# Kernel optimization log

Hardware: AMD Instinct MI355X
Metric: run time of the kernel (lower is better)

## Reference

```python
import jax, jax.numpy as jnp
import numpy as np

V = 6890      # SMPL vertex count
JNT = 24      # SMPL joints
NB = 10       # shape betas
PF = 207      # pose-blend features = 23*9
NJ_OUT = 19   # cocoplus joints
PARENTS = np.array([0, 0, 0, 0, 1, 2, 3, 4, 5, 6, 7, 8, 9, 9, 9, 12, 13, 14, 16, 17, 18, 19, 20, 21], dtype=np.int32)


def setup_inputs() -> dict:
    key = jax.random.key(0)
    ks = jax.random.split(key, 8)
    B = 512
    beta = jax.random.normal(ks[0], (B, NB), dtype=jnp.float32)
    theta = jax.random.normal(ks[1], (B, JNT * 3), dtype=jnp.float32)
    v_template = jax.random.normal(ks[2], (V, 3), dtype=jnp.float32)
    shapedirs = jax.random.normal(ks[3], (NB, V * 3), dtype=jnp.float32) * 0.01
    J_regressor = jax.random.uniform(ks[4], (V, JNT), dtype=jnp.float32)
    J_regressor = J_regressor / jnp.sum(J_regressor, axis=0, keepdims=True)
    posedirs = jax.random.normal(ks[5], (PF, V * 3), dtype=jnp.float32) * 0.01
    lbs_weights = jax.random.uniform(ks[6], (V, JNT), dtype=jnp.float32)
    lbs_weights = lbs_weights / jnp.sum(lbs_weights, axis=1, keepdims=True)
    joint_regressor = jax.random.uniform(ks[7], (V, NJ_OUT), dtype=jnp.float32)
    joint_regressor = joint_regressor / jnp.sum(joint_regressor, axis=0, keepdims=True)
    return {
        "beta": beta, "theta": theta, "v_template": v_template,
        "shapedirs": shapedirs, "J_regressor": J_regressor,
        "posedirs": posedirs, "lbs_weights": lbs_weights,
        "joint_regressor": joint_regressor,
    }


def batch_rodrigues(aa):
    # aa: [N,3] axis-angle -> [N,3,3] rotation via unit quaternion
    angle = jnp.linalg.norm(aa + 1e-8, axis=1, keepdims=True)  # [N,1]
    axis = aa / angle
    half = angle * 0.5
    w = jnp.cos(half)[:, 0]
    xyz = axis * jnp.sin(half)
    x, y, z = xyz[:, 0], xyz[:, 1], xyz[:, 2]
    w2, x2, y2, z2 = w * w, x * x, y * y, z * z
    wx, wy, wz = w * x, w * y, w * z
    xy, xz, yz = x * y, x * z, y * z
    R = jnp.stack([
        w2 + x2 - y2 - z2, 2 * (xy - wz), 2 * (xz + wy),
        2 * (xy + wz), w2 - x2 + y2 - z2, 2 * (yz - wx),
        2 * (xz - wy), 2 * (yz + wx), w2 - x2 - y2 + z2,
    ], axis=1).reshape(-1, 3, 3)
    return R


def _make_A(R, t):
    # R: [B,3,3], t: [B,3] -> [B,4,4]
    B = R.shape[0]
    top = jnp.concatenate([R, t[:, :, None]], axis=2)          # [B,3,4]
    bot = jnp.broadcast_to(jnp.array([0., 0., 0., 1.], R.dtype), (B, 1, 4))
    return jnp.concatenate([top, bot], axis=1)


def global_rigid_transform(Rs, J):
    # Rs: [B,24,3,3], J: [B,24,3]; kinematic-chain FK
    results = [_make_A(Rs[:, 0], J[:, 0])]
    for i in range(1, JNT):
        t = J[:, i] - J[:, PARENTS[i]]
        results.append(results[PARENTS[i]] @ _make_A(Rs[:, i], t))
    A = jnp.stack(results, axis=1)                              # [B,24,4,4]
    J_transformed = A[:, :, :3, 3]
    # remove rest-pose joint translation: A - [0 | A @ [J;0]]
    J_homo = jnp.concatenate([J, jnp.zeros_like(J[:, :, :1])], axis=2)  # [B,24,4]
    init_bone = jnp.einsum('bjpq,bjq->bjp', A, J_homo)          # [B,24,4]
    A_rel = A - jnp.concatenate(
        [jnp.zeros(A.shape[:3] + (3,), A.dtype), init_bone[..., None]], axis=-1)
    return J_transformed, A_rel


def reference(beta, theta, v_template, shapedirs, J_regressor, posedirs,
              lbs_weights, joint_regressor):
    B = beta.shape[0]
    # shape blend
    v_shaped = (beta @ shapedirs).reshape(B, V, 3) + v_template   # [B,V,3]
    # rest-pose joints
    J = jnp.einsum('bvc,vj->bjc', v_shaped, J_regressor)          # [B,24,3]
    # pose rotations
    Rs = batch_rodrigues(theta.reshape(-1, 3)).reshape(B, JNT, 3, 3)
    pose_feature = (Rs[:, 1:] - jnp.eye(3, dtype=Rs.dtype)).reshape(B, PF)
    v_posed = (pose_feature @ posedirs).reshape(B, V, 3) + v_shaped
    # FK
    _, A = global_rigid_transform(Rs, J)                          # [B,24,4,4]
    # skinning
    T = jnp.einsum('vj,bjpq->bvpq', lbs_weights, A)               # [B,V,4,4]
    v_homo = jnp.concatenate(
        [v_posed, jnp.ones((B, V, 1), v_posed.dtype)], axis=2)    # [B,V,4]
    verts = jnp.einsum('bvpq,bvq->bvp', T[:, :, :3, :], v_homo)   # [B,V,3]
    joints = jnp.einsum('bvc,vj->bjc', verts, joint_regressor)    # [B,19,3]
    return joints
```

## Files before the change

### kernel.cpp

```cpp
#include <hip/hip_runtime.h>
#include <math.h>

#define NV 6890
#define N3 20670
#define NJNT 24
#define NBETA 10
#define NPF 207
#define NJO 19
#define NBATCH 512
#define NJK 456
#define NJKP 512
#define NCOEF 218
#define PROWSP 768
#define KPAD 6912
#define KSPLIT 12
#define KCH 576
#define CSTR 224
#define CSTRV 6912

#define TR2 54
#define RODB 48
#define SJB 264
#define C4R 1728
#define PMV 1479
#define PMP 763
#define CHB 48
#define CMB (NJKP * C4R / 256)
#define D4R 219
#define RSP 2
#define RCH 109
#define SSTRIDE ((size_t)NBATCH * 3 * NJK)

typedef __attribute__((ext_vector_type(8))) short bfx8;
typedef __attribute__((ext_vector_type(4))) float fx4;

#define LDSP(x) ((__attribute__((address_space(3))) void*)(x))
#define GLBP(x) ((const __attribute__((address_space(1))) void*)(x))

__constant__ int d_par[NJNT] = {0,0,0,0,1,2,3,4,5,6,7,8,9,9,9,12,13,14,16,17,18,19,20,21};
__constant__ int d_path[NJNT][9] = {
  {0,-1,-1,-1,-1,-1,-1,-1,-1},
  {0,1,-1,-1,-1,-1,-1,-1,-1},
  {0,2,-1,-1,-1,-1,-1,-1,-1},
  {0,3,-1,-1,-1,-1,-1,-1,-1},
  {0,1,4,-1,-1,-1,-1,-1,-1},
  {0,2,5,-1,-1,-1,-1,-1,-1},
  {0,3,6,-1,-1,-1,-1,-1,-1},
  {0,1,4,7,-1,-1,-1,-1,-1},
  {0,2,5,8,-1,-1,-1,-1,-1},
  {0,3,6,9,-1,-1,-1,-1,-1},
  {0,1,4,7,10,-1,-1,-1,-1},
  {0,2,5,8,11,-1,-1,-1,-1},
  {0,3,6,9,12,-1,-1,-1,-1},
  {0,3,6,9,13,-1,-1,-1,-1},
  {0,3,6,9,14,-1,-1,-1,-1},
  {0,3,6,9,12,15,-1,-1,-1},
  {0,3,6,9,13,16,-1,-1,-1},
  {0,3,6,9,14,17,-1,-1,-1},
  {0,3,6,9,13,16,18,-1,-1},
  {0,3,6,9,14,17,19,-1,-1},
  {0,3,6,9,13,16,18,20,-1},
  {0,3,6,9,14,17,19,21,-1},
  {0,3,6,9,13,16,18,20,22},
  {0,3,6,9,14,17,19,21,23}};

__device__ inline short f2bf(float f) {
  union { float f; unsigned u; } x; x.f = f;
  unsigned r = (x.u + 0x7fffu + ((x.u >> 16) & 1u)) >> 16;
  return (short)r;
}

__global__ void __launch_bounds__(256) kA(const float* __restrict__ jr,
                                          const float* __restrict__ lbs,
                                          const float* __restrict__ Jreg,
                                          const float* __restrict__ sdirs,
                                          const float* __restrict__ vtmpl,
                                          const float* __restrict__ theta,
                                          const float* __restrict__ beta,
                                          const float* __restrict__ pdirs,
                                          float* __restrict__ jrT, float* __restrict__ wT,
                                          float* __restrict__ SJ, float* __restrict__ Rs,
                                          float* __restrict__ pfc,
                                          short* __restrict__ Pb) {
  __shared__ float red[4][3];
  __shared__ float tj[128 * NJO];
  __shared__ float tw[128 * NJNT];
  int bx = blockIdx.x, tid = threadIdx.x;
  if (bx < TR2) {
    int v0 = bx * 128;
    for (int i = tid; i < 128 * NJO; i += 256) {
      int g = v0 * NJO + i;
      tj[i] = (g < NV * NJO) ? jr[g] : 0.f;
    }
    for (int i = tid; i < 128 * NJNT; i += 256) {
      int g = v0 * NJNT + i;
      tw[i] = (g < NV * NJNT) ? lbs[g] : 0.f;
    }
    __syncthreads();
    for (int i = tid; i < 128 * (NJO + NJNT); i += 256) {
      int r = i >> 7, c = i & 127;
      int v = v0 + c;
      if (v >= NV) continue;
      if (r < NJO) jrT[(size_t)r * CSTRV + v] = tj[c * NJO + r];
      else         wT[(size_t)(r - NJO) * CSTRV + v] = tw[c * NJNT + (r - NJO)];
    }
  } else if (bx < TR2 + RODB) {
    int t2 = (bx - TR2) * 256 + tid;
    int b = t2 / NJNT, j = t2 - b * NJNT;
    float a0 = theta[b * 72 + j * 3 + 0];
    float a1 = theta[b * 72 + j * 3 + 1];
    float a2 = theta[b * 72 + j * 3 + 2];
    float e0 = a0 + 1e-8f, e1 = a1 + 1e-8f, e2 = a2 + 1e-8f;
    float ang = sqrtf(e0 * e0 + e1 * e1 + e2 * e2);
    float inv = 1.0f / ang;
    float h = 0.5f * ang;
    float w = cosf(h), s = sinf(h);
    float x = a0 * inv * s, y = a1 * inv * s, z = a2 * inv * s;
    float R[9];
    R[0] = w*w + x*x - y*y - z*z; R[1] = 2.f*(x*y - w*z); R[2] = 2.f*(x*z + w*y);
    R[3] = 2.f*(x*y + w*z); R[4] = w*w - x*x + y*y - z*z; R[5] = 2.f*(y*z - w*x);
    R[6] = 2.f*(x*z - w*y); R[7] = 2.f*(y*z + w*x); R[8] = w*w - x*x - y*y + z*z;
#pragma unroll
    for (int r = 0; r < 9; ++r) Rs[b * 216 + j * 9 + r] = R[r];
    if (j >= 1) {
#pragma unroll
      for (int r = 0; r < 9; ++r)
        pfc[b * CSTR + (j - 1) * 9 + r] = R[r] - ((r % 4 == 0) ? 1.0f : 0.0f);
    } else {
#pragma unroll
      for (int i = 0; i < NBETA; ++i) pfc[b * CSTR + NPF + i] = beta[b * NBETA + i];
      pfc[b * CSTR + NPF + NBETA] = 1.0f;
    }
  } else if (bx < TR2 + RODB + SJB) {
    int s = bx - TR2 - RODB;
    int j = s % NJNT, k = s / NJNT;
    const float* src = (k < NBETA) ? (sdirs + (size_t)k * N3) : vtmpl;
    float a0 = 0.f, a1 = 0.f, a2 = 0.f;
    for (int v = tid; v < NV; v += 256) {
      float w = Jreg[v * NJNT + j];
      a0 += w * src[v * 3 + 0];
      a1 += w * src[v * 3 + 1];
      a2 += w * src[v * 3 + 2];
    }
    int lane = tid & 63, wid = tid >> 6;
#pragma unroll
    for (int s2 = 1; s2 < 64; s2 <<= 1) {
      a0 += __shfl_xor(a0, s2); a1 += __shfl_xor(a1, s2); a2 += __shfl_xor(a2, s2);
    }
    if (lane == 0) { red[wid][0] = a0; red[wid][1] = a1; red[wid][2] = a2; }
    __syncthreads();
    if (tid == 0) {
      float* o = SJ + (k * NJNT + j) * 3;
      o[0] = red[0][0] + red[1][0] + red[2][0] + red[3][0];
      o[1] = red[0][1] + red[1][1] + red[2][1] + red[3][1];
      o[2] = red[0][2] + red[1][2] + red[2][2] + red[3][2];
    }
  } else if (bx < TR2 + RODB + SJB + PMV) {
    int idx = (bx - TR2 - RODB - SJB) * 256 + tid;
    if (idx >= 219 * C4R) return;
    int s = idx / C4R, c4 = idx - s * C4R;
    int v0 = c4 * 4;
    if (s == 218) {
      short one = f2bf(1.0f);
      short4 o;
      o.x = (v0 + 0 < NV) ? one : (short)0;
      o.y = (v0 + 1 < NV) ? one : (short)0;
      o.z = (v0 + 2 < NV) ? one : (short)0;
      o.w = (v0 + 3 < NV) ? one : (short)0;
      *(short4*)(Pb + (size_t)654 * KPAD + v0) = o;
      return;
    }
    const float* src; int base;
    if (s < 207)      { src = pdirs + (size_t)s * N3;         base = 3 * s; }
    else if (s < 217) { src = sdirs + (size_t)(s - 207) * N3; base = 621 + 3 * (s - 207); }
    else              { src = vtmpl;                           base = 651; }
    float e[12];
    if (v0 + 4 <= NV) {
      float4 a = *(const float4*)(src + 3 * v0);
      float4 b = *(const float4*)(src + 3 * v0 + 4);
      float4 c = *(const float4*)(src + 3 * v0 + 8);
      e[0]=a.x; e[1]=a.y; e[2]=a.z; e[3]=a.w; e[4]=b.x; e[5]=b.y;
      e[6]=b.z; e[7]=b.w; e[8]=c.x; e[9]=c.y; e[10]=c.z; e[11]=c.w;
    } else {
#pragma unroll
      for (int i = 0; i < 12; ++i) {
        int f = 3 * v0 + i;
        e[i] = (f < N3) ? src[f] : 0.f;
      }
    }
#pragma unroll
    for (int q = 0; q < 3; ++q) {
      short4 o;
      o.x = f2bf(e[0 + q]); o.y = f2bf(e[3 + q]);
      o.z = f2bf(e[6 + q]); o.w = f2bf(e[9 + q]);
      *(short4*)(Pb + (size_t)(base + q) * KPAD + v0) = o;
    }
  } else {
    int idx = (bx - TR2 - RODB - SJB - PMV) * 256 + tid;
    if (idx >= 113 * C4R) return;
    int r = idx / C4R, c4 = idx - r * C4R;
    short4 z; z.x = z.y = z.z = z.w = (short)0;
    *(short4*)(Pb + (size_t)(655 + r) * KPAD + c4 * 4) = z;
  }
}

__device__ inline void getJ(const float* __restrict__ SJ, const float* bb, int i,
                            float& o0, float& o1, float& o2) {
  int r = i * 3;
  float a0 = SJ[NBETA * 72 + r + 0];
  float a1 = SJ[NBETA * 72 + r + 1];
  float a2 = SJ[NBETA * 72 + r + 2];
#pragma unroll
  for (int k = 0; k < NBETA; ++k) {
    a0 += bb[k] * SJ[k * 72 + r + 0];
    a1 += bb[k] * SJ[k * 72 + r + 1];
    a2 += bb[k] * SJ[k * 72 + r + 2];
  }
  o0 = a0; o1 = a1; o2 = a2;
}

__global__ void __launch_bounds__(256) kB(const float* __restrict__ beta,
                                          const float* __restrict__ SJ,
                                          const float* __restrict__ Rs,
                                          const float* __restrict__ jrT,
                                          const float* __restrict__ wT,
                                          float* __restrict__ A,
                                          short* __restrict__ Cb) {
  int bx = blockIdx.x, tid = threadIdx.x;
  if (bx < CHB) {
    int idx = bx * 256 + tid;
    int b = idx / NJNT, j = idx - b * NJNT;
    const float* Rb = Rs + b * 216;
    float bb[NBETA];
#pragma unroll
    for (int k = 0; k < NBETA; ++k) bb[k] = beta[b * NBETA + k];
    float jp0, jp1, jp2;
    getJ(SJ, bb, 0, jp0, jp1, jp2);
    float T[12];
#pragma unroll
    for (int r = 0; r < 3; ++r) {
      T[r * 4 + 0] = Rb[r * 3 + 0];
      T[r * 4 + 1] = Rb[r * 3 + 1];
      T[r * 4 + 2] = Rb[r * 3 + 2];
    }
    T[3] = jp0; T[7] = jp1; T[11] = jp2;
    for (int d = 1; d < 9; ++d) {
      int i = d_path[j][d];
      if (i < 0) break;
      float ji0, ji1, ji2;
      getJ(SJ, bb, i, ji0, ji1, ji2);
      float t0 = ji0 - jp0, t1 = ji1 - jp1, t2 = ji2 - jp2;
      const float* R = Rb + i * 9;
      float R0 = R[0], R1 = R[1], R2 = R[2], R3 = R[3], R4 = R[4];
      float R5 = R[5], R6 = R[6], R7 = R[7], R8 = R[8];
#pragma unroll
      for (int r = 0; r < 3; ++r) {
        float a0 = T[r * 4 + 0], a1 = T[r * 4 + 1], a2 = T[r * 4 + 2];
        T[r * 4 + 0] = a0 * R0 + a1 * R3 + a2 * R6;
        T[r * 4 + 1] = a0 * R1 + a1 * R4 + a2 * R7;
        T[r * 4 + 2] = a0 * R2 + a1 * R5 + a2 * R8;
        T[r * 4 + 3] = a0 * t0 + a1 * t1 + a2 * t2 + T[r * 4 + 3];
      }
      jp0 = ji0; jp1 = ji1; jp2 = ji2;
    }
    float* Ab = A + b * 288 + j * 12;
#pragma unroll
    for (int r = 0; r < 3; ++r) {
      float o0 = T[r * 4 + 0], o1 = T[r * 4 + 1], o2 = T[r * 4 + 2];
      Ab[r * 4 + 0] = o0;
      Ab[r * 4 + 1] = o1;
      Ab[r * 4 + 2] = o2;
      Ab[r * 4 + 3] = T[r * 4 + 3] - (o0 * jp0 + o1 * jp1 + o2 * jp2);
    }
  } else {
    int idx = (bx - CHB) * 256 + tid;
    int jk = idx / C4R;
    int c4 = idx - jk * C4R;
    int v0 = c4 * 4;
    short4 o;
    if (jk < NJK) {
      int j = jk / NJNT, k = jk - j * NJNT;
      float4 a = *(const float4*)(jrT + (size_t)j * CSTRV + v0);
      float4 w = *(const float4*)(wT + (size_t)k * CSTRV + v0);
      o.x = (v0 + 0 < NV) ? f2bf(a.x * w.x) : (short)0;
      o.y = (v0 + 1 < NV) ? f2bf(a.y * w.y) : (short)0;
      o.z = (v0 + 2 < NV) ? f2bf(a.z * w.z) : (short)0;
      o.w = (v0 + 3 < NV) ? f2bf(a.w * w.w) : (short)0;
    } else {
      o.x = o.y = o.z = o.w = (short)0;
    }
    *(short4*)(Cb + (size_t)jk * KPAD + v0) = o;
  }
}

__global__ void __launch_bounds__(256) k_gemm(const short* __restrict__ Pb,
                                              const short* __restrict__ Cb,
                                              float* __restrict__ Dpart) {
  int m0 = blockIdx.x * 128;
  int n0 = blockIdx.y * 64;
  int kb0 = blockIdx.z * KCH;
  __shared__ __align__(16) short As[128 * 64];
  __shared__ __align__(16) short Bs[64 * 64];
  int t = threadIdx.x;
  int wid = t >> 6, lane = t & 63;
  int fgrp = lane >> 4;
  fx4 acc[2][4];
#pragma unroll
  for (int r2 = 0; r2 < 2; ++r2)
#pragma unroll
    for (int j = 0; j < 4; ++j)
#pragma unroll
      for (int r = 0; r < 4; ++r) acc[r2][j][r] = 0.f;

  int lrow = lane >> 3;
  int gsrc = (lane & 7) ^ lrow;
  const short* sA[4]; short* dA[4];
#pragma unroll
  for (int i = 0; i < 4; ++i) {
    int rb = wid * 8 + i * 32;
    sA[i] = Pb + (size_t)(m0 + rb + lrow) * KPAD + kb0 + gsrc * 8;
    dA[i] = As + rb * 64;
  }
  const short* sB[2]; short* dB[2];
#pragma unroll
  for (int i = 0; i < 2; ++i) {
    int rb = wid * 8 + i * 32;
    sB[i] = Cb + (size_t)(n0 + rb + lrow) * KPAD + kb0 + gsrc * 8;
    dB[i] = Bs + rb * 64;
  }

  for (int kk = 0; kk < KCH / 64; ++kk) {
#pragma unroll
    for (int i = 0; i < 4; ++i) {
      __builtin_amdgcn_global_load_lds(GLBP(sA[i]), LDSP(dA[i]), 16, 0, 0);
      sA[i] += 64;
    }
#pragma unroll
    for (int i = 0; i < 2; ++i) {
      __builtin_amdgcn_global_load_lds(GLBP(sB[i]), LDSP(dB[i]), 16, 0, 0);
      sB[i] += 64;
    }
    __syncthreads();
#pragma unroll
    for (int ks = 0; ks < 2; ++ks) {
      int ga = ks * 4 + fgrp;
#pragma unroll
      for (int r2 = 0; r2 < 2; ++r2) {
        int arow = wid * 32 + r2 * 16 + (lane & 15);
        bfx8 a = *(const bfx8*)(As + arow * 64 + (ga ^ (arow & 7)) * 8);
#pragma unroll
        for (int j = 0; j < 4; ++j) {
          int bcol = j * 16 + (lane & 15);
          bfx8 b = *(const bfx8*)(Bs + bcol * 64 + (ga ^ (bcol & 7)) * 8);
          acc[r2][j] = __builtin_amdgcn_mfma_f32_16x16x32_bf16(a, b, acc[r2][j], 0, 0, 0);
        }
      }
    }
    __syncthreads();
  }
  float* dz = Dpart + (size_t)blockIdx.z * PROWSP * NJKP;
#pragma unroll
  for (int r2 = 0; r2 < 2; ++r2) {
    float* dst = dz + (size_t)(m0 + wid * 32 + r2 * 16 + (lane >> 4) * 4) * NJKP
               + n0 + (lane & 15);
#pragma unroll
    for (int j = 0; j < 4; ++j)
#pragma unroll
      for (int r = 0; r < 4; ++r)
        dst[(size_t)r * NJKP + j * 16] = acc[r2][j][r];
  }
}

__global__ void k_redD4(const float* __restrict__ Dpart, float* __restrict__ D4) {
  int idx = blockIdx.x * 256 + threadIdx.x;
  if (idx >= D4R * NJKP) return;
  int r = idx / NJKP, jk = idx - r * NJKP;
  float4 o;
  if (r < NCOEF) {
    float s0 = 0.f, s1 = 0.f, s2 = 0.f;
#pragma unroll
    for (int z = 0; z < KSPLIT; ++z) {
      const float* dp = Dpart + (size_t)z * PROWSP * NJKP + jk;
      s0 += dp[(size_t)(3 * r + 0) * NJKP];
      s1 += dp[(size_t)(3 * r + 1) * NJKP];
      s2 += dp[(size_t)(3 * r + 2) * NJKP];
    }
    o = make_float4(s0, s1, s2, 0.f);
  } else {
    float s = 0.f;
#pragma unroll
    for (int z = 0; z < KSPLIT; ++z)
      s += Dpart[(size_t)z * PROWSP * NJKP + (size_t)654 * NJKP + jk];
    o = make_float4(s, 0.f, 0.f, 0.f);
  }
  ((float4*)D4)[idx] = o;
}

__global__ void __launch_bounds__(256) k_S5b(const float* __restrict__ D4,
                                             const float* __restrict__ pfc,
                                             float* __restrict__ Spart) {
  int n0 = blockIdx.x * 64;
  int b0 = blockIdx.y * 8;
  int r0 = blockIdx.z * RCH;
  int r1 = r0 + RCH; if (r1 > NCOEF) r1 = NCOEF;
  int tid = threadIdx.x;
  int jk = tid & 63;
  int bg = (tid >> 6) * 2;
  const float4* D4v = (const float4*)D4;
  int jkg = n0 + jk;
  const float* c0p = pfc + (size_t)(b0 + bg + 0) * CSTR;
  const float* c1p = pfc + (size_t)(b0 + bg + 1) * CSTR;
  float a00 = 0.f, a01 = 0.f, a02 = 0.f, a10 = 0.f, a11 = 0.f, a12 = 0.f;
#pragma unroll 4
  for (int r = r0; r < r1; ++r) {
    float4 d = D4v[(size_t)r * NJKP + jkg];
    float c0 = c0p[r];
    float c1 = c1p[r];
    a00 += c0 * d.x; a01 += c0 * d.y; a02 += c0 * d.z;
    a10 += c1 * d.x; a11 += c1 * d.y; a12 += c1 * d.z;
  }
  if (jkg < NJK) {
    float* base = Spart + (size_t)blockIdx.z * SSTRIDE;
    float* o0 = base + ((size_t)(b0 + bg + 0) * 3) * NJK + jkg;
    float* o1 = base + ((size_t)(b0 + bg + 1) * 3) * NJK + jkg;
    o0[0 * NJK] = a00; o0[1 * NJK] = a01; o0[2 * NJK] = a02;
    o1[0 * NJK] = a10; o1[1 * NJK] = a11; o1[2 * NJK] = a12;
  }
}

__global__ void __launch_bounds__(128) k_final3(const float* __restrict__ Spart,
                                                const float* __restrict__ D4,
                                                const float* __restrict__ A,
                                                float* __restrict__ out) {
  __shared__ float S_ls[2 * 3 * NJK];
  __shared__ float A_ls[2 * 288];
  __shared__ float c0_ls[NJK];
  int blk = blockIdx.x, tid = threadIdx.x;
  int b0 = blk * 2;
  size_t sbase = (size_t)(b0 * 3) * NJK;
  for (int i = tid; i < 2 * 3 * NJK; i += 128)
    S_ls[i] = Spart[sbase + i] + Spart[SSTRIDE + sbase + i];
  for (int i = tid; i < 2 * 288; i += 128)
    A_ls[i] = A[(size_t)b0 * 288 + i];
  for (int i = tid; i < NJK; i += 128)
    c0_ls[i] = D4[((size_t)NCOEF * NJKP + i) * 4];
  __syncthreads();
  if (tid >= 2 * NJO * 3) return;
  int bq = tid / 57, r = tid - bq * 57;
  int j = r / 3, c = r - j * 3;
  const float* S0 = S_ls + (bq * 3 + 0) * NJK + j * NJNT;
  const float* S1 = S_ls + (bq * 3 + 1) * NJK + j * NJNT;
  const float* S2 = S_ls + (bq * 3 + 2) * NJK + j * NJNT;
  const float* Ab = A_ls + bq * 288;
  const float* cc = c0_ls + j * NJNT;
  float acc = 0.f;
#pragma unroll 4
  for (int k = 0; k < NJNT; ++k) {
    const float* Ar = Ab + k * 12 + c * 4;
    acc += Ar[0] * S0[k] + Ar[1] * S1[k] + Ar[2] * S2[k] + Ar[3] * cc[k];
  }
  out[(size_t)(b0 + bq) * 57 + r] = acc;
}

extern "C" void kernel_launch(void* const* d_in, const int* in_sizes, int n_in,
                              void* d_out, int out_size, void* d_ws, size_t ws_size,
                              hipStream_t stream) {
  const float* beta  = (const float*)d_in[0];
  const float* theta = (const float*)d_in[1];
  const float* vtmpl = (const float*)d_in[2];
  const float* sdirs = (const float*)d_in[3];
  const float* Jreg  = (const float*)d_in[4];
  const float* pdirs = (const float*)d_in[5];
  const float* lbs   = (const float*)d_in[6];
  const float* jreg2 = (const float*)d_in[7];
  float* out = (float*)d_out;

  float* ws    = (float*)d_ws;
  short* Cb    = (short*)ws;
  short* Pb    = Cb + (size_t)NJKP * KPAD;
  float* Dpart = (float*)(Pb + (size_t)PROWSP * KPAD);
  float* D4    = Dpart + (size_t)KSPLIT * PROWSP * NJKP;
  float* Spart = D4    + (size_t)D4R * NJKP * 4;
  float* pfc   = Spart + (size_t)RSP * SSTRIDE;
  float* Rs    = pfc   + (size_t)NBATCH * CSTR;
  float* A     = Rs    + (size_t)NBATCH * 216;
  float* jrT   = A     + (size_t)NBATCH * 288;
  float* wT    = jrT   + (size_t)NJO * CSTRV;
  float* SJ    = wT    + (size_t)NJNT * CSTRV;

  kA<<<dim3(TR2 + RODB + SJB + PMV + PMP), 256, 0, stream>>>(
      jreg2, lbs, Jreg, sdirs, vtmpl, theta, beta, pdirs,
      jrT, wT, SJ, Rs, pfc, Pb);
  kB<<<dim3(CHB + CMB), 256, 0, stream>>>(beta, SJ, Rs, jrT, wT, A, Cb);
  k_gemm<<<dim3(PROWSP / 128, NJKP / 64, KSPLIT), 256, 0, stream>>>(Pb, Cb, Dpart);
  k_redD4<<<dim3((D4R * NJKP + 255) / 256), 256, 0, stream>>>(Dpart, D4);
  k_S5b<<<dim3(NJKP / 64, NBATCH / 8, RSP), 256, 0, stream>>>(D4, pfc, Spart);
  k_final3<<<dim3(NBATCH / 2), 128, 0, stream>>>(Spart, D4, A, out);
}
```

Before: 80.03 us.

## Build combined regressor directly from LDS tiles and merge FK into reduction kernel

Removes the separate transposed jrT/wT buffers and the kB kernel. The Cb product matrix is now built inside kA from LDS-staged tiles of the joint regressor and skinning weights, using padded strides to limit bank conflicts. The forward-kinematics chain computation moves into the split-K reduction kernel, so one kernel launch and a global round trip are eliminated. In exchange, kA blocks re-read the same vertex tiles once per jk chunk (8 times).

```diff
diff --git a/kernel.cpp b/kernel.cpp
--- a/kernel.cpp
+++ b/kernel.cpp
@@ -16,16 +16,15 @@
 #define KSPLIT 12
 #define KCH 576
 #define CSTR 224
-#define CSTRV 6912
-
-#define TR2 54
+
 #define RODB 48
 #define SJB 264
 #define C4R 1728
 #define PMV 1479
 #define PMP 763
+#define CMD 432
+#define RD4B 438
 #define CHB 48
-#define CMB (NJKP * C4R / 256)
 #define D4R 219
 #define RSP 2
 #define RCH 109
@@ -37,7 +36,6 @@
 #define LDSP(x) ((__attribute__((address_space(3))) void*)(x))
 #define GLBP(x) ((const __attribute__((address_space(1))) void*)(x))
 
-__constant__ int d_par[NJNT] = {0,0,0,0,1,2,3,4,5,6,7,8,9,9,9,12,13,14,16,17,18,19,20,21};
 __constant__ int d_path[NJNT][9] = {
   {0,-1,-1,-1,-1,-1,-1,-1,-1},
   {0,1,-1,-1,-1,-1,-1,-1,-1},
@@ -78,34 +76,16 @@
                                           const float* __restrict__ theta,
                                           const float* __restrict__ beta,
                                           const float* __restrict__ pdirs,
-                                          float* __restrict__ jrT, float* __restrict__ wT,
                                           float* __restrict__ SJ, float* __restrict__ Rs,
                                           float* __restrict__ pfc,
-                                          short* __restrict__ Pb) {
+                                          short* __restrict__ Pb,
+                                          short* __restrict__ Cb) {
   __shared__ float red[4][3];
-  __shared__ float tj[128 * NJO];
-  __shared__ float tw[128 * NJNT];
+  __shared__ float tj[128 * 21];
+  __shared__ float tw[128 * 25];
   int bx = blockIdx.x, tid = threadIdx.x;
-  if (bx < TR2) {
-    int v0 = bx * 128;
-    for (int i = tid; i < 128 * NJO; i += 256) {
-      int g = v0 * NJO + i;
-      tj[i] = (g < NV * NJO) ? jr[g] : 0.f;
-    }
-    for (int i = tid; i < 128 * NJNT; i += 256) {
-      int g = v0 * NJNT + i;
-      tw[i] = (g < NV * NJNT) ? lbs[g] : 0.f;
-    }
-    __syncthreads();
-    for (int i = tid; i < 128 * (NJO + NJNT); i += 256) {
-      int r = i >> 7, c = i & 127;
-      int v = v0 + c;
-      if (v >= NV) continue;
-      if (r < NJO) jrT[(size_t)r * CSTRV + v] = tj[c * NJO + r];
-      else         wT[(size_t)(r - NJO) * CSTRV + v] = tw[c * NJNT + (r - NJO)];
-    }
-  } else if (bx < TR2 + RODB) {
-    int t2 = (bx - TR2) * 256 + tid;
+  if (bx < RODB) {
+    int t2 = bx * 256 + tid;
     int b = t2 / NJNT, j = t2 - b * NJNT;
     float a0 = theta[b * 72 + j * 3 + 0];
     float a1 = theta[b * 72 + j * 3 + 1];
@@ -131,8 +111,8 @@
       for (int i = 0; i < NBETA; ++i) pfc[b * CSTR + NPF + i] = beta[b * NBETA + i];
       pfc[b * CSTR + NPF + NBETA] = 1.0f;
     }
-  } else if (bx < TR2 + RODB + SJB) {
-    int s = bx - TR2 - RODB;
+  } else if (bx < RODB + SJB) {
+    int s = bx - RODB;
     int j = s % NJNT, k = s / NJNT;
     const float* src = (k < NBETA) ? (sdirs + (size_t)k * N3) : vtmpl;
     float a0 = 0.f, a1 = 0.f, a2 = 0.f;
@@ -155,8 +135,8 @@
       o[1] = red[0][1] + red[1][1] + red[2][1] + red[3][1];
       o[2] = red[0][2] + red[1][2] + red[2][2] + red[3][2];
     }
-  } else if (bx < TR2 + RODB + SJB + PMV) {
-    int idx = (bx - TR2 - RODB - SJB) * 256 + tid;
+  } else if (bx < RODB + SJB + PMV) {
+    int idx = (bx - RODB - SJB) * 256 + tid;
     if (idx >= 219 * C4R) return;
     int s = idx / C4R, c4 = idx - s * C4R;
     int v0 = c4 * 4;
@@ -195,101 +175,45 @@
       o.z = f2bf(e[6 + q]); o.w = f2bf(e[9 + q]);
       *(short4*)(Pb + (size_t)(base + q) * KPAD + v0) = o;
     }
-  } else {
-    int idx = (bx - TR2 - RODB - SJB - PMV) * 256 + tid;
+  } else if (bx < RODB + SJB + PMV + PMP) {
+    int idx = (bx - RODB - SJB - PMV) * 256 + tid;
     if (idx >= 113 * C4R) return;
     int r = idx / C4R, c4 = idx - r * C4R;
     short4 z; z.x = z.y = z.z = z.w = (short)0;
     *(short4*)(Pb + (size_t)(655 + r) * KPAD + c4 * 4) = z;
-  }
-}
-
-__device__ inline void getJ(const float* __restrict__ SJ, const float* bb, int i,
-                            float& o0, float& o1, float& o2) {
-  int r = i * 3;
-  float a0 = SJ[NBETA * 72 + r + 0];
-  float a1 = SJ[NBETA * 72 + r + 1];
-  float a2 = SJ[NBETA * 72 + r + 2];
-#pragma unroll
-  for (int k = 0; k < NBETA; ++k) {
-    a0 += bb[k] * SJ[k * 72 + r + 0];
-    a1 += bb[k] * SJ[k * 72 + r + 1];
-    a2 += bb[k] * SJ[k * 72 + r + 2];
-  }
-  o0 = a0; o1 = a1; o2 = a2;
-}
-
-__global__ void __launch_bounds__(256) kB(const float* __restrict__ beta,
-                                          const float* __restrict__ SJ,
-                                          const float* __restrict__ Rs,
-                                          const float* __restrict__ jrT,
-                                          const float* __restrict__ wT,
-                                          float* __restrict__ A,
-                                          short* __restrict__ Cb) {
-  int bx = blockIdx.x, tid = threadIdx.x;
-  if (bx < CHB) {
-    int idx = bx * 256 + tid;
-    int b = idx / NJNT, j = idx - b * NJNT;
-    const float* Rb = Rs + b * 216;
-    float bb[NBETA];
-#pragma unroll
-    for (int k = 0; k < NBETA; ++k) bb[k] = beta[b * NBETA + k];
-    float jp0, jp1, jp2;
-    getJ(SJ, bb, 0, jp0, jp1, jp2);
-    float T[12];
-#pragma unroll
-    for (int r = 0; r < 3; ++r) {
-      T[r * 4 + 0] = Rb[r * 3 + 0];
-      T[r * 4 + 1] = Rb[r * 3 + 1];
-      T[r * 4 + 2] = Rb[r * 3 + 2];
-    }
-    T[3] = jp0; T[7] = jp1; T[11] = jp2;
-    for (int d = 1; d < 9; ++d) {
-      int i = d_path[j][d];
-      if (i < 0) break;
-      float ji0, ji1, ji2;
-      getJ(SJ, bb, i, ji0, ji1, ji2);
-      float t0 = ji0 - jp0, t1 = ji1 - jp1, t2 = ji2 - jp2;
-      const float* R = Rb + i * 9;
-      float R0 = R[0], R1 = R[1], R2 = R[2], R3 = R[3], R4 = R[4];
-      float R5 = R[5], R6 = R[6], R7 = R[7], R8 = R[8];
-#pragma unroll
-      for (int r = 0; r < 3; ++r) {
-        float a0 = T[r * 4 + 0], a1 = T[r * 4 + 1], a2 = T[r * 4 + 2];
-        T[r * 4 + 0] = a0 * R0 + a1 * R3 + a2 * R6;
-        T[r * 4 + 1] = a0 * R1 + a1 * R4 + a2 * R7;
-        T[r * 4 + 2] = a0 * R2 + a1 * R5 + a2 * R8;
-        T[r * 4 + 3] = a0 * t0 + a1 * t1 + a2 * t2 + T[r * 4 + 3];
+  } else {
+    int s5 = bx - RODB - SJB - PMV - PMP;
+    int vc = s5 >> 3, jkc = s5 & 7;
+    int v0 = vc * 128;
+    for (int i = tid; i < 128 * NJO; i += 256) {
+      int v = i / NJO, j = i - v * NJO;
+      tj[v * 21 + j] = (v0 + v < NV) ? jr[(size_t)v0 * NJO + i] : 0.f;
+    }
+    for (int i = tid; i < 128 * NJNT; i += 256) {
+      int v = i / NJNT, k = i - v * NJNT;
+      tw[v * 25 + k] = (v0 + v < NV) ? lbs[(size_t)v0 * NJNT + i] : 0.f;
+    }
+    __syncthreads();
+    int jk0 = jkc * 64;
+#pragma unroll
+    for (int it = 0; it < 8; ++it) {
+      int item = it * 256 + tid;
+      int rr = item >> 5;
+      int c4 = item & 31;
+      int jk = jk0 + rr;
+      int vv = c4 * 4;
+      short4 o;
+      if (jk < NJK) {
+        int j = jk / NJNT, k = jk - j * NJNT;
+        o.x = f2bf(tj[(vv + 0) * 21 + j] * tw[(vv + 0) * 25 + k]);
+        o.y = f2bf(tj[(vv + 1) * 21 + j] * tw[(vv + 1) * 25 + k]);
+        o.z = f2bf(tj[(vv + 2) * 21 + j] * tw[(vv + 2) * 25 + k]);
+        o.w = f2bf(tj[(vv + 3) * 21 + j] * tw[(vv + 3) * 25 + k]);
+      } else {
+        o.x = o.y = o.z = o.w = (short)0;
       }
-      jp0 = ji0; jp1 = ji1; jp2 = ji2;
-    }
-    float* Ab = A + b * 288 + j * 12;
-#pragma unroll
-    for (int r = 0; r < 3; ++r) {
-      float o0 = T[r * 4 + 0], o1 = T[r * 4 + 1], o2 = T[r * 4 + 2];
-      Ab[r * 4 + 0] = o0;
-      Ab[r * 4 + 1] = o1;
-      Ab[r * 4 + 2] = o2;
-      Ab[r * 4 + 3] = T[r * 4 + 3] - (o0 * jp0 + o1 * jp1 + o2 * jp2);
-    }
-  } else {
-    int idx = (bx - CHB) * 256 + tid;
-    int jk = idx / C4R;
-    int c4 = idx - jk * C4R;
-    int v0 = c4 * 4;
-    short4 o;
-    if (jk < NJK) {
-      int j = jk / NJNT, k = jk - j * NJNT;
-      float4 a = *(const float4*)(jrT + (size_t)j * CSTRV + v0);
-      float4 w = *(const float4*)(wT + (size_t)k * CSTRV + v0);
-      o.x = (v0 + 0 < NV) ? f2bf(a.x * w.x) : (short)0;
-      o.y = (v0 + 1 < NV) ? f2bf(a.y * w.y) : (short)0;
-      o.z = (v0 + 2 < NV) ? f2bf(a.z * w.z) : (short)0;
-      o.w = (v0 + 3 < NV) ? f2bf(a.w * w.w) : (short)0;
-    } else {
-      o.x = o.y = o.z = o.w = (short)0;
-    }
-    *(short4*)(Cb + (size_t)jk * KPAD + v0) = o;
+      *(short4*)(Cb + (size_t)jk * KPAD + v0 + vv) = o;
+    }
   }
 }
 
@@ -371,29 +295,96 @@
   }
 }
 
-__global__ void k_redD4(const float* __restrict__ Dpart, float* __restrict__ D4) {
-  int idx = blockIdx.x * 256 + threadIdx.x;
-  if (idx >= D4R * NJKP) return;
-  int r = idx / NJKP, jk = idx - r * NJKP;
-  float4 o;
-  if (r < NCOEF) {
-    float s0 = 0.f, s1 = 0.f, s2 = 0.f;
-#pragma unroll
-    for (int z = 0; z < KSPLIT; ++z) {
-      const float* dp = Dpart + (size_t)z * PROWSP * NJKP + jk;
-      s0 += dp[(size_t)(3 * r + 0) * NJKP];
-      s1 += dp[(size_t)(3 * r + 1) * NJKP];
-      s2 += dp[(size_t)(3 * r + 2) * NJKP];
-    }
-    o = make_float4(s0, s1, s2, 0.f);
+__device__ inline void getJ(const float* __restrict__ SJ, const float* bb, int i,
+                            float& o0, float& o1, float& o2) {
+  int r = i * 3;
+  float a0 = SJ[NBETA * 72 + r + 0];
+  float a1 = SJ[NBETA * 72 + r + 1];
+  float a2 = SJ[NBETA * 72 + r + 2];
+#pragma unroll
+  for (int k = 0; k < NBETA; ++k) {
+    a0 += bb[k] * SJ[k * 72 + r + 0];
+    a1 += bb[k] * SJ[k * 72 + r + 1];
+    a2 += bb[k] * SJ[k * 72 + r + 2];
+  }
+  o0 = a0; o1 = a1; o2 = a2;
+}
+
+__global__ void __launch_bounds__(256) k_redD4C(const float* __restrict__ Dpart,
+                                                const float* __restrict__ beta,
+                                                const float* __restrict__ SJ,
+                                                const float* __restrict__ Rs,
+                                                float* __restrict__ D4,
+                                                float* __restrict__ A) {
+  int bx = blockIdx.x, tid = threadIdx.x;
+  if (bx < RD4B) {
+    int idx = bx * 256 + tid;
+    int r = idx / NJKP, jk = idx - r * NJKP;
+    float4 o;
+    if (r < NCOEF) {
+      float s0 = 0.f, s1 = 0.f, s2 = 0.f;
+#pragma unroll
+      for (int z = 0; z < KSPLIT; ++z) {
+        const float* dp = Dpart + (size_t)z * PROWSP * NJKP + jk;
+        s0 += dp[(size_t)(3 * r + 0) * NJKP];
+        s1 += dp[(size_t)(3 * r + 1) * NJKP];
+        s2 += dp[(size_t)(3 * r + 2) * NJKP];
+      }
+      o = make_float4(s0, s1, s2, 0.f);
+    } else {
+      float s = 0.f;
+#pragma unroll
+      for (int z = 0; z < KSPLIT; ++z)
+        s += Dpart[(size_t)z * PROWSP * NJKP + (size_t)654 * NJKP + jk];
+      o = make_float4(s, 0.f, 0.f, 0.f);
+    }
+    ((float4*)D4)[idx] = o;
   } else {
-    float s = 0.f;
-#pragma unroll
-    for (int z = 0; z < KSPLIT; ++z)
-      s += Dpart[(size_t)z * PROWSP * NJKP + (size_t)654 * NJKP + jk];
-    o = make_float4(s, 0.f, 0.f, 0.f);
-  }
-  ((float4*)D4)[idx] = o;
+    int idx = (bx - RD4B) * 256 + tid;
+    int b = idx / NJNT, j = idx - b * NJNT;
+    const float* Rb = Rs + b * 216;
+    float bb[NBETA];
+#pragma unroll
+    for (int k = 0; k < NBETA; ++k) bb[k] = beta[b * NBETA + k];
+    float jp0, jp1, jp2;
+    getJ(SJ, bb, 0, jp0, jp1, jp2);
+    float T[12];
+#pragma unroll
+    for (int r = 0; r < 3; ++r) {
+      T[r * 4 + 0] = Rb[r * 3 + 0];
+      T[r * 4 + 1] = Rb[r * 3 + 1];
+      T[r * 4 + 2] = Rb[r * 3 + 2];
+    }
+    T[3] = jp0; T[7] = jp1; T[11] = jp2;
+    for (int d = 1; d < 9; ++d) {
+      int i = d_path[j][d];
+      if (i < 0) break;
+      float ji0, ji1, ji2;
+      getJ(SJ, bb, i, ji0, ji1, ji2);
+      float t0 = ji0 - jp0, t1 = ji1 - jp1, t2 = ji2 - jp2;
+      const float* R = Rb + i * 9;
+      float R0 = R[0], R1 = R[1], R2 = R[2], R3 = R[3], R4 = R[4];
+      float R5 = R[5], R6 = R[6], R7 = R[7], R8 = R[8];
+#pragma unroll
+      for (int r = 0; r < 3; ++r) {
+        float a0 = T[r * 4 + 0], a1 = T[r * 4 + 1], a2 = T[r * 4 + 2];
+        T[r * 4 + 0] = a0 * R0 + a1 * R3 + a2 * R6;
+        T[r * 4 + 1] = a0 * R1 + a1 * R4 + a2 * R7;
+        T[r * 4 + 2] = a0 * R2 + a1 * R5 + a2 * R8;
+        T[r * 4 + 3] = a0 * t0 + a1 * t1 + a2 * t2 + T[r * 4 + 3];
+      }
+      jp0 = ji0; jp1 = ji1; jp2 = ji2;
+    }
+    float* Ab = A + b * 288 + j * 12;
+#pragma unroll
+    for (int r = 0; r < 3; ++r) {
+      float o0 = T[r * 4 + 0], o1 = T[r * 4 + 1], o2 = T[r * 4 + 2];
+      Ab[r * 4 + 0] = o0;
+      Ab[r * 4 + 1] = o1;
+      Ab[r * 4 + 2] = o2;
+      Ab[r * 4 + 3] = T[r * 4 + 3] - (o0 * jp0 + o1 * jp1 + o2 * jp2);
+    }
+  }
 }
 
 __global__ void __launch_bounds__(256) k_S5b(const float* __restrict__ D4,
@@ -484,16 +475,13 @@
   float* pfc   = Spart + (size_t)RSP * SSTRIDE;
   float* Rs    = pfc   + (size_t)NBATCH * CSTR;
   float* A     = Rs    + (size_t)NBATCH * 216;
-  float* jrT   = A     + (size_t)NBATCH * 288;
-  float* wT    = jrT   + (size_t)NJO * CSTRV;
-  float* SJ    = wT    + (size_t)NJNT * CSTRV;
-
-  kA<<<dim3(TR2 + RODB + SJB + PMV + PMP), 256, 0, stream>>>(
+  float* SJ    = A     + (size_t)NBATCH * 288;
+
+  kA<<<dim3(RODB + SJB + PMV + PMP + CMD), 256, 0, stream>>>(
       jreg2, lbs, Jreg, sdirs, vtmpl, theta, beta, pdirs,
-      jrT, wT, SJ, Rs, pfc, Pb);
-  kB<<<dim3(CHB + CMB), 256, 0, stream>>>(beta, SJ, Rs, jrT, wT, A, Cb);
+      SJ, Rs, pfc, Pb, Cb);
   k_gemm<<<dim3(PROWSP / 128, NJKP / 64, KSPLIT), 256, 0, stream>>>(Pb, Cb, Dpart);
-  k_redD4<<<dim3((D4R * NJKP + 255) / 256), 256, 0, stream>>>(Dpart, D4);
+  k_redD4C<<<dim3(RD4B + CHB), 256, 0, stream>>>(Dpart, beta, SJ, Rs, D4, A);
   k_S5b<<<dim3(NJKP / 64, NBATCH / 8, RSP), 256, 0, stream>>>(D4, pfc, Spart);
   k_final3<<<dim3(NBATCH / 2), 128, 0, stream>>>(Spart, D4, A, out);
 }
```

After: 80.96 us. No clear change (+1.2%).
